# Kernel optimization log

Hardware: AMD Instinct MI355X
Metric: run time of the kernel (lower is better)

The kernel has to match this reference:

```python
import jax, jax.numpy as jnp
import numpy as np

B, K, C, HEADS, R, N, FF = 8, 512, 256, 8, 4, 64, 1024
HT = 2 * R + 1  # rel-pos table side = 9


def layer_norm(x, g, b, eps=1e-5):
    mu = jnp.mean(x, axis=-1, keepdims=True)
    var = jnp.var(x, axis=-1, keepdims=True)
    return (x - mu) * jax.lax.rsqrt(var + eps) * g + b


def grid_sample_table(table, grid):
    """Bilinear grid_sample, align_corners=True, zeros padding.
    table: [heads, H, W] (batch-expanded in torch, identical per batch)
    grid:  [b, k, n, 2] in [-1, 1]  ->  out [b, heads, k, n]
    """
    heads, H, W = table.shape
    gx = (grid[..., 0] + 1.0) * 0.5 * (W - 1)
    gy = (grid[..., 1] + 1.0) * 0.5 * (H - 1)
    x0 = jnp.floor(gx); y0 = jnp.floor(gy)
    x1 = x0 + 1.0;      y1 = y0 + 1.0
    wx1 = gx - x0; wx0 = 1.0 - wx1
    wy1 = gy - y0; wy0 = 1.0 - wy1
    flat = table.reshape(heads, H * W)

    def corner(yi, xi, w):
        valid = (xi >= 0) & (xi <= W - 1) & (yi >= 0) & (yi <= H - 1)
        idx = (jnp.clip(yi, 0, H - 1) * W + jnp.clip(xi, 0, W - 1)).astype(jnp.int32)
        return flat[:, idx] * jnp.where(valid, w, 0.0)[None]  # [heads,b,k,n]

    out = (corner(y0, x0, wy0 * wx0) + corner(y0, x1, wy0 * wx1)
           + corner(y1, x0, wy1 * wx0) + corner(y1, x1, wy1 * wx1))
    return jnp.moveaxis(out, 0, 1)  # [b, heads, k, n]


def setup_inputs() -> dict:
    key = jax.random.key(0)
    ks = jax.random.split(key, 16)
    s = 1.0 / np.sqrt(C)
    inp = {
        "query": jax.random.normal(ks[0], (B, K, C), jnp.float32),
        "local_feat": jax.random.normal(ks[1], (B, C, K, N), jnp.float32),
        "local_spat": jax.random.uniform(ks[2], (B, K, N, 2), jnp.float32) * 2.0 - 1.0,
        # rel-pos table is zeros-initialized in torch; use small randn so it's non-trivial
        "rel_table": jax.random.normal(ks[3], (HEADS, HT, HT), jnp.float32) * 0.02,
        "Wq": jax.random.normal(ks[4], (C, C), jnp.float32) * s,
        "bq": jnp.zeros((C,), jnp.float32),
        "Wk": jax.random.normal(ks[5], (C, C), jnp.float32) * s,
        "bk": jnp.zeros((C,), jnp.float32),
        "Wv": jax.random.normal(ks[6], (C, C), jnp.float32) * s,
        "bv": jnp.zeros((C,), jnp.float32),
        "Wo": jax.random.normal(ks[7], (C, C), jnp.float32) * s,
        "bo": jnp.zeros((C,), jnp.float32),
        "ln1_g": jnp.ones((C,), jnp.float32),
        "ln1_b": jnp.zeros((C,), jnp.float32),
        "W1": jax.random.normal(ks[8], (C, FF), jnp.float32) * s,
        "b1": jnp.zeros((FF,), jnp.float32),
        "W2": jax.random.normal(ks[9], (FF, C), jnp.float32) * (1.0 / np.sqrt(FF)),
        "b2": jnp.zeros((C,), jnp.float32),
        "ln2_g": jnp.ones((C,), jnp.float32),
        "ln2_b": jnp.zeros((C,), jnp.float32),
    }
    return inp


def reference(query, local_feat, local_spat, rel_table, Wq, bq, Wk, bk, Wv, bv,
              Wo, bo, ln1_g, ln1_b, W1, b1, W2, b2, ln2_g, ln2_b):
    b, k, c = query.shape
    heads = rel_table.shape[0]
    d = c // heads
    n = local_feat.shape[-1]
    # spatial_score: grid_sample of rel-pos table at per-key offsets -> attention bias
    bias = grid_sample_table(rel_table, local_spat)      # [b, heads, k, n]
    bias = jnp.transpose(bias, (0, 2, 1, 3))             # [b, k, heads, n]
    # local bilateral attention (query attends to its n local samples)
    q = (query @ Wq + bq).reshape(b, k, heads, d)
    feats = jnp.transpose(local_feat, (0, 2, 3, 1))      # [b, k, n, c]
    Kp = (feats @ Wk + bk).reshape(b, k, n, heads, d)
    Vp = (feats @ Wv + bv).reshape(b, k, n, heads, d)
    scores = jnp.einsum('bkhd,bknhd->bkhn', q, Kp) / jnp.sqrt(jnp.float32(d)) + bias
    attn = jax.nn.softmax(scores, axis=-1)
    ctx = jnp.einsum('bkhn,bknhd->bkhd', attn, Vp).reshape(b, k, c)
    x = layer_norm(query + ctx @ Wo + bo, ln1_g, ln1_b)
    h = jax.nn.gelu(x @ W1 + b1) @ W2 + b2
    out = layer_norm(x + h, ln2_g, ln2_b)
    # num_local_scales == 1: stack+mean over scales is identity
    return out
```

## Files before the change

kernel.cpp:

```cpp
#include <hip/hip_runtime.h>
#include <hip/hip_bf16.h>

typedef __hip_bfloat16 bf16;
typedef __attribute__((ext_vector_type(8))) short short8;
typedef __attribute__((ext_vector_type(4))) float float4_;

#define DEV static __device__ __forceinline__

DEV float blo(unsigned w){ return __uint_as_float(w << 16); }
DEV float bhi(unsigned w){ return __uint_as_float(w & 0xffff0000u); }
DEV unsigned short f2bu(float x){ bf16 h = __float2bfloat16(x); unsigned short u; __builtin_memcpy(&u, &h, 2); return u; }
DEV unsigned pack2(float a, float b){ return (unsigned)f2bu(a) | ((unsigned)f2bu(b) << 16); }

DEV float gelu_tanh(float x){
  float z = 0.7978845608028654f * (x + 0.044715f * x * x * x);
  float th = 2.0f / (1.0f + __expf(-2.0f * z)) - 1.0f;
  return 0.5f * x * (1.0f + th);
}


__global__ __launch_bounds__(256) void k_prep(
    const float* __restrict__ query, const float* __restrict__ Wq,
    const float* __restrict__ Wk, const float* __restrict__ Wv,
    const float* __restrict__ Wo, const float* __restrict__ W1, const float* __restrict__ W2,
    bf16* __restrict__ query_bf, bf16* __restrict__ WqT, bf16* __restrict__ WkP,
    bf16* __restrict__ WvP, bf16* __restrict__ WoT, bf16* __restrict__ W1T, bf16* __restrict__ W2T)
{
  __shared__ ushort ts[64][72];
  const int t = threadIdx.x;
  const int bx = blockIdx.x;

  if (bx < 160){
    const float* src; bf16* dst; int ldi, ldo, kt, nt;
    if (bx < 16)      { src = Wq; dst = WqT; ldi = 256;  ldo = 256;  kt = bx & 3;        nt = bx >> 2; }
    else if (bx < 32) { src = Wo; dst = WoT; ldi = 256;  ldo = 256;  kt = (bx-16) & 3;   nt = (bx-16) >> 2; }
    else if (bx < 96) { src = W1; dst = W1T; ldi = 1024; ldo = 256;  kt = (bx-32) & 3;   nt = (bx-32) >> 2; }
    else              { src = W2; dst = W2T; ldi = 256;  ldo = 1024; kt = (bx-96) & 15;  nt = (bx-96) >> 4; }
    int k0 = kt * 64, n0 = nt * 64;
    {
      int r = t >> 2, c0 = (t & 3) * 16;
      #pragma unroll
      for (int g = 0; g < 4; g++){
        float4 v = *(const float4*)&src[(size_t)(k0 + r)*ldi + n0 + c0 + g*4];
        ts[r][c0+g*4+0] = f2bu(v.x); ts[r][c0+g*4+1] = f2bu(v.y);
        ts[r][c0+g*4+2] = f2bu(v.z); ts[r][c0+g*4+3] = f2bu(v.w);
      }
    }
    __syncthreads();
    {
      int rr = t >> 2, cc0 = (t & 3) * 16;
      unsigned wbuf[8];
      #pragma unroll
      for (int j = 0; j < 8; j++)
        wbuf[j] = (unsigned)ts[cc0+2*j][rr] | ((unsigned)ts[cc0+2*j+1][rr] << 16);
      uint4* d = (uint4*)(dst + (size_t)(n0 + rr)*ldo + k0 + cc0);
      d[0] = make_uint4(wbuf[0], wbuf[1], wbuf[2], wbuf[3]);
      d[1] = make_uint4(wbuf[4], wbuf[5], wbuf[6], wbuf[7]);
    }
  } else if (bx < 192){
    int idx = bx - 160, h = idx >> 2, kt = idx & 3, k0 = kt * 64;
    {
      int r = t >> 2, d0 = (t & 3) * 8;
      #pragma unroll
      for (int g = 0; g < 2; g++){
        float4 v = *(const float4*)&Wv[(size_t)(k0 + r)*256 + h*32 + d0 + g*4];
        ts[r][d0+g*4+0] = f2bu(v.x); ts[r][d0+g*4+1] = f2bu(v.y);
        ts[r][d0+g*4+2] = f2bu(v.z); ts[r][d0+g*4+3] = f2bu(v.w);
      }
    }
    __syncthreads();
    {
      int d = t >> 3, cc0 = (t & 7) * 8;
      unsigned wbuf[4];
      #pragma unroll
      for (int j = 0; j < 4; j++)
        wbuf[j] = (unsigned)ts[cc0+2*j][d] | ((unsigned)ts[cc0+2*j+1][d] << 16);
      *(uint4*)(WvP + (size_t)h*8192 + (size_t)d*256 + k0 + cc0) =
          make_uint4(wbuf[0], wbuf[1], wbuf[2], wbuf[3]);
    }
  } else if (bx < 200){
    int off = (bx - 192) * 8192;
    #pragma unroll
    for (int g = 0; g < 8; g++){
      int i = off + g*1024 + t*4;
      int h = i >> 13, c = (i >> 5) & 255, d = i & 31;
      float4 v = *(const float4*)&Wk[(size_t)c*256 + h*32 + d];
      *(uint2*)(WkP + i) = make_uint2(pack2(v.x, v.y), pack2(v.z, v.w));
    }
  } else {
    int off = (bx - 200) * 16384;
    #pragma unroll
    for (int g = 0; g < 16; g++){
      int i = off + g*1024 + t*4;
      float4 v = *(const float4*)&query[i];
      *(uint2*)(query_bf + i) = make_uint2(pack2(v.x, v.y), pack2(v.z, v.w));
    }
  }
}

template<int KDIM, int NT, int EPI>
__global__ __launch_bounds__(256) void k_gemm(
    const bf16* __restrict__ A, int lda, int acolH,
    const bf16* __restrict__ BT, int btH,
    const float* __restrict__ bias,
    bf16* __restrict__ Cb, int ldc, int ncolH)
{
  constexpr int KB = (KDIM >= 64) ? 64 : 32;
  constexpr int LP = KB + 8;
  constexpr int ASEG = KB / 8;
  __shared__ short As[64][LP];
  __shared__ short Bs[NT][LP];

  const int t = threadIdx.x;
  const int w = t >> 6, l = t & 63, lm = l & 15, lq = l >> 4;
  const int m0 = blockIdx.x * 64;
  const int h = blockIdx.z;
  const size_t acol = (size_t)h * acolH;
  const bf16* Bt = BT + (size_t)h * btH + (size_t)(blockIdx.y * NT) * KDIM;
  const int ncol = h * ncolH + blockIdx.y * NT;

  float4_ acc[NT/16];
  #pragma unroll
  for (int i = 0; i < NT/16; i++) acc[i] = (float4_){0.f,0.f,0.f,0.f};

  for (int k0 = 0; k0 < KDIM; k0 += KB){
    if (k0) __syncthreads();
    for (int i = t; i < 64*ASEG; i += 256){
      int row = i / ASEG, seg = i % ASEG;
      uint4 v = *(const uint4*)(A + (size_t)(m0+row)*lda + acol + k0 + seg*8);
      *(uint4*)&As[row][seg*8] = v;
    }
    for (int i = t; i < NT*ASEG; i += 256){
      int row = i / ASEG, seg = i % ASEG;
      uint4 v = *(const uint4*)(Bt + (size_t)row*KDIM + k0 + seg*8);
      *(uint4*)&Bs[row][seg*8] = v;
    }
    __syncthreads();
    #pragma unroll
    for (int kk = 0; kk < KB/32; kk++){
      short8 af = *(const short8*)&As[w*16 + lm][kk*32 + lq*8];
      #pragma unroll
      for (int nt = 0; nt < NT/16; nt++){
        short8 bfr = *(const short8*)&Bs[nt*16 + lm][kk*32 + lq*8];
        acc[nt] = __builtin_amdgcn_mfma_f32_16x16x32_bf16(af, bfr, acc[nt], 0, 0, 0);
      }
    }
  }

  #pragma unroll
  for (int nt = 0; nt < NT/16; nt++){
    int gcol = ncol + nt*16 + lm;
    float bb = bias ? bias[gcol] : 0.0f;
    #pragma unroll
    for (int rg = 0; rg < 4; rg++){
      int row = m0 + w*16 + lq*4 + rg;
      float v = acc[nt][rg] + bb;
      if (EPI == 0) Cb[(size_t)row*ldc + gcol] = __float2bfloat16(v);
      else          Cb[(size_t)row*ldc + gcol] = __float2bfloat16(gelu_tanh(v));
    }
  }
}

template<int KDIM, int WRITE_BF>
__global__ __launch_bounds__(256) void k_gemm_ln(
    const bf16* __restrict__ A, int lda,
    const bf16* __restrict__ BT,
    const float* __restrict__ bias,
    const float* __restrict__ resid,
    const float* __restrict__ gamma, const float* __restrict__ beta,
    float* __restrict__ Cf, bf16* __restrict__ Cb)
{
  constexpr int KB = 64, LP = 72;
  __shared__ short As[16][LP];
  __shared__ short Bs[256][LP];
  __shared__ float2 part[4][16];

  const int t = threadIdx.x;
  const int w = t >> 6, l = t & 63, lm = l & 15, lq = l >> 4;
  const int m0 = blockIdx.x * 16;

  float4_ acc[4];
  #pragma unroll
  for (int i = 0; i < 4; i++) acc[i] = (float4_){0.f,0.f,0.f,0.f};

  for (int k0 = 0; k0 < KDIM; k0 += KB){
    if (k0) __syncthreads();
    if (t < 128){
      int row = t >> 3, seg = t & 7;
      uint4 v = *(const uint4*)(A + (size_t)(m0+row)*lda + k0 + seg*8);
      *(uint4*)&As[row][seg*8] = v;
    }
    for (int i = t; i < 2048; i += 256){
      int row = i >> 3, seg = i & 7;
      uint4 v = *(const uint4*)(BT + (size_t)row*KDIM + k0 + seg*8);
      *(uint4*)&Bs[row][seg*8] = v;
    }
    __syncthreads();
    #pragma unroll
    for (int kk = 0; kk < 2; kk++){
      short8 af = *(const short8*)&As[lm][kk*32 + lq*8];
      #pragma unroll
      for (int nt = 0; nt < 4; nt++){
        short8 bfr = *(const short8*)&Bs[w*64 + nt*16 + lm][kk*32 + lq*8];
        acc[nt] = __builtin_amdgcn_mfma_f32_16x16x32_bf16(af, bfr, acc[nt], 0, 0, 0);
      }
    }
  }

  float v[4][4];
  float s1[4] = {0,0,0,0}, s2[4] = {0,0,0,0};
  #pragma unroll
  for (int nt = 0; nt < 4; nt++){
    int col = w*64 + nt*16 + lm;
    float bb = bias[col];
    #pragma unroll
    for (int rg = 0; rg < 4; rg++){
      int row = m0 + lq*4 + rg;
      float x = acc[nt][rg] + bb + resid[(size_t)row*256 + col];
      v[nt][rg] = x;
      s1[rg] += x; s2[rg] += x*x;
    }
  }
  #pragma unroll
  for (int off = 1; off < 16; off <<= 1){
    #pragma unroll
    for (int rg = 0; rg < 4; rg++){
      s1[rg] += __shfl_xor(s1[rg], off);
      s2[rg] += __shfl_xor(s2[rg], off);
    }
  }
  if (lm == 0){
    #pragma unroll
    for (int rg = 0; rg < 4; rg++)
      part[w][lq*4 + rg] = make_float2(s1[rg], s2[rg]);
  }
  __syncthreads();
  #pragma unroll
  for (int rg = 0; rg < 4; rg++){
    int rl = lq*4 + rg;
    float S1 = part[0][rl].x + part[1][rl].x + part[2][rl].x + part[3][rl].x;
    float S2 = part[0][rl].y + part[1][rl].y + part[2][rl].y + part[3][rl].y;
    float mean = S1 * (1.0f/256.0f);
    float var  = S2 * (1.0f/256.0f) - mean*mean;
    float inv  = rsqrtf(var + 1e-5f);
    #pragma unroll
    for (int nt = 0; nt < 4; nt++){
      int col = w*64 + nt*16 + lm;
      float o = (v[nt][rg] - mean) * inv * gamma[col] + beta[col];
      size_t idx = (size_t)(m0 + rl)*256 + col;
      Cf[idx] = o;
      if (WRITE_BF) Cb[idx] = __float2bfloat16(o);
    }
  }
}

__global__ __launch_bounds__(256) void k_attn(
    const float* __restrict__ local_feat, const float* __restrict__ local_spat,
    const float* __restrict__ rel_table, const bf16* __restrict__ qk,
    bf16* __restrict__ fctx)
{
  __shared__ __attribute__((aligned(16))) ushort fsT[64][256];
  __shared__ __attribute__((aligned(16))) ushort fs[256][64];
  __shared__ __attribute__((aligned(16))) ushort qkb[8][272];
  __shared__ __attribute__((aligned(16))) ushort attnT[16][64];
  __shared__ __attribute__((aligned(16))) float biasS[8][68];
  __shared__ __attribute__((aligned(16))) float s_scT[8][68];

  const int t = threadIdx.x;
  const int r = blockIdx.x;
  const int b = r >> 9, k = r & 511;
  const int w = t >> 6, l = t & 63, lm = l & 15, lq = l >> 4;

  {
    const int cpair = t >> 3;
    const int mrow  = t & 7;
    const int nq8   = mrow * 8;
    #pragma unroll
    for (int p = 0; p < 4; p++){
      int c0 = p*64 + cpair*2, c1 = c0 + 1;
      const float* s0 = local_feat + ((size_t)((b*256 + c0)*512 + k))*64 + nq8;
      const float* s1 = local_feat + ((size_t)((b*256 + c1)*512 + k))*64 + nq8;
      float4 a0 = *(const float4*)(s0);
      float4 a1 = *(const float4*)(s0 + 4);
      float4 b0 = *(const float4*)(s1);
      float4 b1 = *(const float4*)(s1 + 4);
      ushort u0[8] = { f2bu(a0.x), f2bu(a0.y), f2bu(a0.z), f2bu(a0.w),
                       f2bu(a1.x), f2bu(a1.y), f2bu(a1.z), f2bu(a1.w) };
      ushort u1[8] = { f2bu(b0.x), f2bu(b0.y), f2bu(b0.z), f2bu(b0.w),
                       f2bu(b1.x), f2bu(b1.y), f2bu(b1.z), f2bu(b1.w) };
      {
        int sw0 = nq8 ^ ((c0 & 7) << 3);
        int sw1 = nq8 ^ ((c1 & 7) << 3);
        *(uint4*)&fs[c0][sw0] = make_uint4(
            (unsigned)u0[0] | ((unsigned)u0[1]<<16), (unsigned)u0[2] | ((unsigned)u0[3]<<16),
            (unsigned)u0[4] | ((unsigned)u0[5]<<16), (unsigned)u0[6] | ((unsigned)u0[7]<<16));
        *(uint4*)&fs[c1][sw1] = make_uint4(
            (unsigned)u1[0] | ((unsigned)u1[1]<<16), (unsigned)u1[2] | ((unsigned)u1[3]<<16),
            (unsigned)u1[4] | ((unsigned)u1[5]<<16), (unsigned)u1[6] | ((unsigned)u1[7]<<16));
      }
      #pragma unroll
      for (int i = 0; i < 8; i++){
        int key = ((mrow ^ i) & 7) << 3;
        *(unsigned*)&fsT[nq8 + i][c0 ^ key] = (unsigned)u0[i] | ((unsigned)u1[i] << 16);
      }
    }
  }
  {
    uint4 a = *(const uint4*)(qk + (size_t)r * 2048 + t * 8);
    int h = t >> 5, c0 = (t & 31) * 8;
    *(uint4*)&qkb[h][c0] = a;
  }
  if (t < 64){
    float2 sxy = *(const float2*)&local_spat[((size_t)r*64 + t)*2];
    float gx = (sxy.x + 1.0f) * 4.0f, gy = (sxy.y + 1.0f) * 4.0f;
    float x0f = floorf(gx), y0f = floorf(gy);
    int xi0 = (int)x0f, yi0 = (int)y0f;
    float wx1 = gx - x0f, wx0 = 1.0f - wx1;
    float wy1 = gy - y0f, wy0 = 1.0f - wy1;
    int xs[4] = {xi0, xi0 + 1, xi0, xi0 + 1};
    int ys[4] = {yi0, yi0, yi0 + 1, yi0 + 1};
    float wj[4] = {wy0*wx0, wy0*wx1, wy1*wx0, wy1*wx1};
    float ww[4]; int ix[4];
    #pragma unroll
    for (int j = 0; j < 4; j++){
      bool valid = (xs[j] >= 0) && (xs[j] <= 8) && (ys[j] >= 0) && (ys[j] <= 8);
      ix[j] = min(max(ys[j],0),8)*9 + min(max(xs[j],0),8);
      ww[j] = valid ? wj[j] : 0.0f;
    }
    #pragma unroll
    for (int h = 0; h < 8; h++){
      const float* th = rel_table + h*81;
      biasS[h][t] = th[ix[0]]*ww[0] + th[ix[1]]*ww[1] + th[ix[2]]*ww[2] + th[ix[3]]*ww[3];
    }
  }
  __syncthreads();

  {
    float4_ acc = (float4_){0.f,0.f,0.f,0.f};
    const int arow = w*16 + lm;
    const int akey = (((arow >> 3) ^ arow) & 7) << 3;
    #pragma unroll
    for (int ks = 0; ks < 8; ks++){
      short8 af  = *(const short8*)&fsT[arow][(ks*32 + lq*8) ^ akey];
      short8 bfr = *(const short8*)&qkb[lm & 7][ks*32 + lq*8];
      acc = __builtin_amdgcn_mfma_f32_16x16x32_bf16(af, bfr, acc, 0, 0, 0);
    }
    if (lm < 8){
      const float scale = 0.17677669529663687f;
      int n0 = w*16 + lq*4;
      float4 sv;
      sv.x = acc[0]*scale + biasS[lm][n0+0];
      sv.y = acc[1]*scale + biasS[lm][n0+1];
      sv.z = acc[2]*scale + biasS[lm][n0+2];
      sv.w = acc[3]*scale + biasS[lm][n0+3];
      *(float4*)&s_scT[lm][n0] = sv;
    }
  }
  __syncthreads();

  {
    int g = t >> 5, j = t & 31;
    float sc0 = s_scT[g][j], sc1 = s_scT[g][j+32];
    float m = fmaxf(sc0, sc1);
    #pragma unroll
    for (int off = 1; off < 32; off <<= 1) m = fmaxf(m, __shfl_xor(m, off));
    float e0 = __expf(sc0 - m), e1 = __expf(sc1 - m);
    float s = e0 + e1;
    #pragma unroll
    for (int off = 1; off < 32; off <<= 1) s += __shfl_xor(s, off);
    float inv = 1.0f / s;
    ushort p0 = f2bu(e0 * inv), p1 = f2bu(e1 * inv);
    int key = g << 3;
    attnT[g    ][j        ^ key] = p0;
    attnT[g    ][(j + 32) ^ key] = p1;
    attnT[g + 8][j        ^ key] = p0;
    attnT[g + 8][(j + 32) ^ key] = p1;
  }
  __syncthreads();

  {
    const int bkey = (lm & 7) << 3;
    short8 bf0 = *(const short8*)&attnT[lm][(      lq*8) ^ bkey];
    short8 bf1 = *(const short8*)&attnT[lm][(32 + lq*8) ^ bkey];
    #pragma unroll
    for (int ct = 0; ct < 4; ct++){
      int crow = (w*4 + ct)*16 + lm;
      int ckey = (crow & 7) << 3;
      float4_ acc2 = (float4_){0.f,0.f,0.f,0.f};
      short8 af0 = *(const short8*)&fs[crow][(      lq*8) ^ ckey];
      acc2 = __builtin_amdgcn_mfma_f32_16x16x32_bf16(af0, bf0, acc2, 0, 0, 0);
      short8 af1 = *(const short8*)&fs[crow][(32 + lq*8) ^ ckey];
      acc2 = __builtin_amdgcn_mfma_f32_16x16x32_bf16(af1, bf1, acc2, 0, 0, 0);
      if (lm < 8){
        int c = (w*4 + ct)*16 + lq*4;
        size_t base = (size_t)r*2048 + (size_t)lm*256 + c;
        *(uint2*)&fctx[base] = make_uint2(pack2(acc2[0], acc2[1]), pack2(acc2[2], acc2[3]));
      }
    }
  }
}

extern "C" void kernel_launch(void* const* d_in, const int* in_sizes, int n_in,
                              void* d_out, int out_size, void* d_ws, size_t ws_size,
                              hipStream_t stream)
{
  const float* query      = (const float*)d_in[0];
  const float* local_feat = (const float*)d_in[1];
  const float* local_spat = (const float*)d_in[2];
  const float* rel_table  = (const float*)d_in[3];
  const float* Wq  = (const float*)d_in[4];   const float* bq  = (const float*)d_in[5];
  const float* Wk  = (const float*)d_in[6];
  const float* Wv  = (const float*)d_in[8];   const float* bv  = (const float*)d_in[9];
  const float* Wo  = (const float*)d_in[10];  const float* bo  = (const float*)d_in[11];
  const float* g1  = (const float*)d_in[12];  const float* be1 = (const float*)d_in[13];
  const float* W1  = (const float*)d_in[14];  const float* b1  = (const float*)d_in[15];
  const float* W2  = (const float*)d_in[16];  const float* b2  = (const float*)d_in[17];
  const float* g2  = (const float*)d_in[18];  const float* be2 = (const float*)d_in[19];

  char* ws = (char*)d_ws;
  bf16*  qk       = (bf16*)(ws + 0);
  bf16*  fctx     = (bf16*)(ws + 16777216);
  bf16*  query_bf = (bf16*)(ws + 33554432);
  bf16*  q_bf     = (bf16*)(ws + 35651584);
  bf16*  WqT      = (bf16*)(ws + 37748736);
  bf16*  WkP      = (bf16*)(ws + 37879808);
  bf16*  WvP      = (bf16*)(ws + 38010880);
  bf16*  WoT      = (bf16*)(ws + 38141952);
  bf16*  W1T      = (bf16*)(ws + 38273024);
  bf16*  W2T      = (bf16*)(ws + 38797312);
  bf16*  ctx_bf   = (bf16*)(ws + 0);
  float* x        = (float*)(ws + 2097152);
  bf16*  x_bf     = (bf16*)(ws + 6291456);
  bf16*  h1       = (bf16*)(ws + 20971520);
  float* out      = (float*)d_out;

  dim3 blk(256);
  k_prep<<<dim3(264), blk, 0, stream>>>(query, Wq, Wk, Wv, Wo, W1, W2,
                                        query_bf, WqT, WkP, WvP, WoT, W1T, W2T);
  k_gemm<256,64,0><<<dim3(64,4,1), blk, 0, stream>>>(query_bf, 256, 0, WqT, 0, bq, q_bf, 256, 0);
  k_gemm<32,64,0><<<dim3(64,4,8), blk, 0, stream>>>(q_bf, 256, 32, WkP, 8192, nullptr, qk, 2048, 256);
  k_attn<<<dim3(4096), blk, 0, stream>>>(local_feat, local_spat, rel_table, qk, fctx);
  k_gemm<256,32,0><<<dim3(64,1,8), blk, 0, stream>>>(fctx, 2048, 256, WvP, 8192, bv, ctx_bf, 256, 32);
  k_gemm_ln<256,1><<<dim3(256), blk, 0, stream>>>(ctx_bf, 256, WoT, bo, query, g1, be1, x, x_bf);
  k_gemm<256,64,2><<<dim3(64,16,1), blk, 0, stream>>>(x_bf, 256, 0, W1T, 0, b1, h1, 1024, 0);
  k_gemm_ln<1024,0><<<dim3(256), blk, 0, stream>>>(h1, 1024, W2T, b2, x, g2, be2, out, nullptr);
}
```

Baseline: 502.1 us.

## Fold Wq into per-head Wk products to compute qk with one GEMM

Precomputes a combined weight WqkT[h,c,:] = Wq[:,h] · Wk[c,h] and a matching bias in the prep kernel, so the query-key projection becomes a single GEMM from query_bf instead of a Q projection followed by a per-head K-space GEMM. This removes one kernel launch and the round trip of q_bf through memory. In exchange the prep kernel gains 2048 extra blocks of scalar fp32 dot products, and the fused GEMM does more work (K=256 instead of 32 per head output). It also changes rounding, since the product is formed in fp32 and rounded to bf16 once rather than rounding q first.

```diff
diff --git a/kernel.cpp b/kernel.cpp
--- a/kernel.cpp
+++ b/kernel.cpp
@@ -23,19 +23,20 @@
     const float* __restrict__ query, const float* __restrict__ Wq,
     const float* __restrict__ Wk, const float* __restrict__ Wv,
     const float* __restrict__ Wo, const float* __restrict__ W1, const float* __restrict__ W2,
-    bf16* __restrict__ query_bf, bf16* __restrict__ WqT, bf16* __restrict__ WkP,
+    const float* __restrict__ bq,
+    bf16* __restrict__ query_bf, bf16* __restrict__ WqkT, float* __restrict__ bias_qk,
     bf16* __restrict__ WvP, bf16* __restrict__ WoT, bf16* __restrict__ W1T, bf16* __restrict__ W2T)
 {
   __shared__ ushort ts[64][72];
+  __shared__ float wkS[32];
   const int t = threadIdx.x;
   const int bx = blockIdx.x;
 
-  if (bx < 160){
+  if (bx < 144){
     const float* src; bf16* dst; int ldi, ldo, kt, nt;
-    if (bx < 16)      { src = Wq; dst = WqT; ldi = 256;  ldo = 256;  kt = bx & 3;        nt = bx >> 2; }
-    else if (bx < 32) { src = Wo; dst = WoT; ldi = 256;  ldo = 256;  kt = (bx-16) & 3;   nt = (bx-16) >> 2; }
-    else if (bx < 96) { src = W1; dst = W1T; ldi = 1024; ldo = 256;  kt = (bx-32) & 3;   nt = (bx-32) >> 2; }
-    else              { src = W2; dst = W2T; ldi = 256;  ldo = 1024; kt = (bx-96) & 15;  nt = (bx-96) >> 4; }
+    if (bx < 16)      { src = Wo; dst = WoT; ldi = 256;  ldo = 256;  kt = bx & 3;        nt = bx >> 2; }
+    else if (bx < 80) { src = W1; dst = W1T; ldi = 1024; ldo = 256;  kt = (bx-16) & 3;   nt = (bx-16) >> 2; }
+    else              { src = W2; dst = W2T; ldi = 256;  ldo = 1024; kt = (bx-80) & 15;  nt = (bx-80) >> 4; }
     int k0 = kt * 64, n0 = nt * 64;
     {
       int r = t >> 2, c0 = (t & 3) * 16;
@@ -57,8 +58,8 @@
       d[0] = make_uint4(wbuf[0], wbuf[1], wbuf[2], wbuf[3]);
       d[1] = make_uint4(wbuf[4], wbuf[5], wbuf[6], wbuf[7]);
     }
-  } else if (bx < 192){
-    int idx = bx - 160, h = idx >> 2, kt = idx & 3, k0 = kt * 64;
+  } else if (bx < 176){
+    int idx = bx - 144, h = idx >> 2, kt = idx & 3, k0 = kt * 64;
     {
       int r = t >> 2, d0 = (t & 3) * 8;
       #pragma unroll
@@ -78,22 +79,28 @@
       *(uint4*)(WvP + (size_t)h*8192 + (size_t)d*256 + k0 + cc0) =
           make_uint4(wbuf[0], wbuf[1], wbuf[2], wbuf[3]);
     }
-  } else if (bx < 200){
-    int off = (bx - 192) * 8192;
-    #pragma unroll
-    for (int g = 0; g < 8; g++){
-      int i = off + g*1024 + t*4;
-      int h = i >> 13, c = (i >> 5) & 255, d = i & 31;
-      float4 v = *(const float4*)&Wk[(size_t)c*256 + h*32 + d];
-      *(uint2*)(WkP + i) = make_uint2(pack2(v.x, v.y), pack2(v.z, v.w));
-    }
-  } else {
-    int off = (bx - 200) * 16384;
+  } else if (bx < 240){
+    int off = (bx - 176) * 16384;
     #pragma unroll
     for (int g = 0; g < 16; g++){
       int i = off + g*1024 + t*4;
       float4 v = *(const float4*)&query[i];
       *(uint2*)(query_bf + i) = make_uint2(pack2(v.x, v.y), pack2(v.z, v.w));
+    }
+  } else {
+    int idx = bx - 240, h = idx >> 8, c = idx & 255;
+    if (t < 32) wkS[t] = Wk[(size_t)c*256 + h*32 + t];
+    __syncthreads();
+    float acc = 0.f;
+    const float* wq = Wq + (size_t)t*256 + h*32;
+    #pragma unroll
+    for (int d = 0; d < 32; d++) acc += wq[d] * wkS[d];
+    WqkT[(size_t)(h*256 + c)*256 + t] = __float2bfloat16(acc);
+    if (t == 0){
+      float bacc = 0.f;
+      #pragma unroll
+      for (int d = 0; d < 32; d++) bacc += bq[h*32 + d] * wkS[d];
+      bias_qk[h*256 + c] = bacc;
     }
   }
 }
@@ -421,13 +428,12 @@
   bf16*  qk       = (bf16*)(ws + 0);
   bf16*  fctx     = (bf16*)(ws + 16777216);
   bf16*  query_bf = (bf16*)(ws + 33554432);
-  bf16*  q_bf     = (bf16*)(ws + 35651584);
-  bf16*  WqT      = (bf16*)(ws + 37748736);
-  bf16*  WkP      = (bf16*)(ws + 37879808);
-  bf16*  WvP      = (bf16*)(ws + 38010880);
-  bf16*  WoT      = (bf16*)(ws + 38141952);
-  bf16*  W1T      = (bf16*)(ws + 38273024);
-  bf16*  W2T      = (bf16*)(ws + 38797312);
+  bf16*  WqkT     = (bf16*)(ws + 35651584);
+  bf16*  WoT      = (bf16*)(ws + 36700160);
+  bf16*  WvP      = (bf16*)(ws + 36831232);
+  bf16*  W1T      = (bf16*)(ws + 36962304);
+  bf16*  W2T      = (bf16*)(ws + 37486592);
+  float* bias_qk  = (float*)(ws + 38010880);
   bf16*  ctx_bf   = (bf16*)(ws + 0);
   float* x        = (float*)(ws + 2097152);
   bf16*  x_bf     = (bf16*)(ws + 6291456);
@@ -435,10 +441,9 @@
   float* out      = (float*)d_out;
 
   dim3 blk(256);
-  k_prep<<<dim3(264), blk, 0, stream>>>(query, Wq, Wk, Wv, Wo, W1, W2,
-                                        query_bf, WqT, WkP, WvP, WoT, W1T, W2T);
-  k_gemm<256,64,0><<<dim3(64,4,1), blk, 0, stream>>>(query_bf, 256, 0, WqT, 0, bq, q_bf, 256, 0);
-  k_gemm<32,64,0><<<dim3(64,4,8), blk, 0, stream>>>(q_bf, 256, 32, WkP, 8192, nullptr, qk, 2048, 256);
+  k_prep<<<dim3(2288), blk, 0, stream>>>(query, Wq, Wk, Wv, Wo, W1, W2, bq,
+                                         query_bf, WqkT, bias_qk, WvP, WoT, W1T, W2T);
+  k_gemm<256,64,0><<<dim3(64,32,1), blk, 0, stream>>>(query_bf, 256, 0, WqkT, 0, bias_qk, qk, 2048, 0);
   k_attn<<<dim3(4096), blk, 0, stream>>>(local_feat, local_spat, rel_table, qk, fctx);
   k_gemm<256,32,0><<<dim3(64,1,8), blk, 0, stream>>>(fctx, 2048, 256, WvP, 8192, bv, ctx_bf, 256, 32);
   k_gemm_ln<256,1><<<dim3(256), blk, 0, stream>>>(ctx_bf, 256, WoT, bo, query, g1, be1, x, x_bf);
```

After: 506.0 us. No clear change (+0.8%).
